# Optimization experiments

Hardware: AMD Instinct MI355X
Metric: run time of the kernel (lower is better)

## Reference

```python
import jax, jax.numpy as jnp
import numpy as np

SEQ_LEN = 720
PRED_LEN = 720
CHANNELS = 321
CUT_FREQ = 200
FREQ_OUT = 400  # int(cut_freq * (seq_len+pred_len)/seq_len)
LENGTH_RATIO = (SEQ_LEN + PRED_LEN) / SEQ_LEN  # 2.0
BATCH = 256


def setup_inputs() -> dict:
    key = jax.random.key(0)
    ks = jax.random.split(key, 8)
    scale = 1.0 / np.sqrt(CUT_FREQ)  # Linear-style init scale
    return {
        "x_enc": jax.random.normal(ks[0], (BATCH, SEQ_LEN, CHANNELS), dtype=jnp.float32),
        "x_mark_enc": jax.random.normal(ks[1], (BATCH, SEQ_LEN, 4), dtype=jnp.float32),
        "x_dec": jax.random.normal(ks[2], (BATCH, PRED_LEN, CHANNELS), dtype=jnp.float32),
        "x_mark_dec": jax.random.normal(ks[3], (BATCH, PRED_LEN, 4), dtype=jnp.float32),
        "Wr": jax.random.normal(ks[4], (CHANNELS, FREQ_OUT, CUT_FREQ), dtype=jnp.float32) * scale,
        "Wi": jax.random.normal(ks[5], (CHANNELS, FREQ_OUT, CUT_FREQ), dtype=jnp.float32) * scale,
        "br": jax.random.normal(ks[6], (CHANNELS, FREQ_OUT), dtype=jnp.float32) * scale,
        "bi": jax.random.normal(ks[7], (CHANNELS, FREQ_OUT), dtype=jnp.float32) * scale,
    }


def reference(x_enc, x_mark_enc, x_dec, x_mark_dec, Wr, Wi, br, bi):
    # RevIN-style normalization along time dim (unbiased variance, as torch.var)
    x_mean = jnp.mean(x_enc, axis=1, keepdims=True)                 # [B,1,C]
    x = x_enc - x_mean
    x_var = jnp.var(x, axis=1, keepdims=True, ddof=1)               # [B,1,C]
    x_stdev = jnp.sqrt(x_var + 1e-5)
    x = x / x_stdev

    # Low-pass in frequency domain
    x_freq = jnp.fft.rfft(x, axis=1)                                # [B, S//2+1, C] complex
    x_freq_low = x_freq[:, :CUT_FREQ, :]                            # [B, F_in, C]

    # Per-channel complex linear (the python loop over channels fused into one einsum)
    W = (Wr + 1j * Wi).astype(jnp.complex64)                        # [C, F_out, F_in]
    b = (br + 1j * bi).astype(jnp.complex64)                        # [C, F_out]
    out_freq = jnp.einsum('bfc,cof->boc', x_freq_low, W) + b.T[None]  # [B, F_out, C]

    # Back to time domain at the upsampled length
    total = SEQ_LEN + PRED_LEN
    out = jnp.fft.irfft(out_freq, n=total, axis=1) * LENGTH_RATIO   # [B, S+P, C]
    out = out[:, -PRED_LEN:, :]

    # De-normalize
    return out * x_stdev + x_mean
```

## Files before the change

kernel.cpp:

```cpp
#include <hip/hip_runtime.h>
#include <math.h>

#define SEQ    720
#define PRED   720
#define CH     321
#define FCUT   200
#define FOUT   400
#define NBATCH 256
#define NTOT   1440
#define KR     400
#define MC     800

typedef _Float16 f16;
typedef f16   f16x8 __attribute__((ext_vector_type(8)));
typedef float f32x4 __attribute__((ext_vector_type(4)));

static __device__ __forceinline__ f32x4 mfma16(f16x8 a, f16x8 b, f32x4 c) {
    return __builtin_amdgcn_mfma_f32_16x16x32_f16(a, b, c, 0, 0, 0);
}
static __device__ __forceinline__ f16 tof16(float v) { return (f16)v; }
static __device__ __forceinline__ ushort f16bits(f16 h) { return __builtin_bit_cast(unsigned short, h); }
static __device__ __forceinline__ f16 bits2f16(ushort u) { return __builtin_bit_cast(f16, u); }

__global__ void init_dmat(f16* __restrict__ Dh, f16* __restrict__ Dl) {
    int i = blockIdx.x * 256 + threadIdx.x;
    if (i >= KR * SEQ) return;
    int fp = i / SEQ, t = i % SEQ;
    int f = (fp < FCUT) ? fp : (fp - FCUT);
    int p = (f * t) % SEQ;
    float ang = (float)p * (6.28318530717958647692f / (float)SEQ);
    float v = (fp < FCUT) ? cosf(ang) : -sinf(ang);
    f16 h = tof16(v);
    Dh[i] = h;
    Dl[i] = tof16(v - (float)h);
}

__global__ void init_gmat(f16* __restrict__ Gh, f16* __restrict__ Gl) {
    int i = blockIdx.x * 256 + threadIdx.x;
    if (i >= SEQ * MC) return;
    int tp = i / MC, kp = i % MC;
    int t = tp + PRED;
    int k = (kp < FOUT) ? kp : (kp - FOUT);
    int p = (k * t) % NTOT;
    float ang = (float)p * (6.28318530717958647692f / (float)NTOT);
    const float s = 2.0f / (float)NTOT;
    float v;
    if (kp < FOUT) v = (k == 0) ? s : (2.0f * s * cosf(ang));
    else           v = (k == 0) ? 0.0f : (-2.0f * s * sinf(ang));
    f16 h = tof16(v);
    Gh[i] = h;
    Gl[i] = tof16(v - (float)h);
}

__global__ void stats_kernel(const float* __restrict__ x,
                             float* __restrict__ mean_bc,
                             float* __restrict__ rstd_bc,
                             float* __restrict__ stdev_bc) {
    int i = blockIdx.x * 256 + threadIdx.x;
    if (i >= NBATCH * CH) return;
    int b = i / CH, c = i % CH;
    const float* p = x + (size_t)b * SEQ * CH + c;
    float s = 0.f, ss = 0.f;
    for (int t = 0; t < SEQ; ++t) {
        float v = p[(size_t)t * CH];
        s += v; ss += v * v;
    }
    float mean = s / (float)SEQ;
    float var = fmaxf((ss - s * mean) / (float)(SEQ - 1), 0.f);
    float st = sqrtf(var + 1e-5f);
    mean_bc[i] = mean;
    stdev_bc[i] = st;
    rstd_bc[i] = 1.0f / st;
}

template<int MODE>
__global__ __launch_bounds__(256)
void gemm_mfma(const f16* __restrict__ Ahg,
               const f16* __restrict__ Alg,
               const void* __restrict__ Bg,
               void* __restrict__ Cg,
               const float* __restrict__ P0,
               const float* __restrict__ P1,
               const float* __restrict__ P2,
               const float* __restrict__ P3,
               int Bc, int b0, int gx, int gy)
{
    const int M   = (MODE == 0) ? KR : (MODE == 1) ? MC : SEQ;
    const int K   = (MODE == 0) ? SEQ : (MODE == 1) ? KR : MC;
    const int N   = (MODE == 0) ? CH : Bc;
    const int ldb = (MODE == 0) ? CH : Bc;
    const int ldc = (MODE == 0) ? CH : Bc;

    int orig = blockIdx.x;
    int q = (int)gridDim.x >> 3, r = (int)gridDim.x & 7, xcd = orig & 7;
    int id = (xcd < r ? xcd * (q + 1) : r * (q + 1) + (xcd - r) * q) + (orig >> 3);

    const int z   = id / (gx * gy);
    const int rem = id - z * (gx * gy);
    const int my  = rem / gx;
    const int mx  = rem - my * gx;
    const int m0  = mx * 128;
    const int n0  = my * 128;

    const void* Bp = nullptr; void* Cp = nullptr;
    const float* wrc = nullptr; const float* wic = nullptr;
    const float* mnp = nullptr; const float* rsp = nullptr;
    if (MODE == 0) {
        int b = b0 + z;
        Bp  = (const float*)Bg + (size_t)b * SEQ * CH;
        Cp  = (ushort*)Cg + (size_t)z * KR * CH;
        mnp = P0 + (size_t)b * CH;
        rsp = P1 + (size_t)b * CH;
    } else if (MODE == 1) {
        Bp  = (const ushort*)Bg + (size_t)z * KR * Bc;
        Cp  = (ushort*)Cg + (size_t)z * MC * Bc;
        wrc = P0 + (size_t)z * FOUT * FCUT;
        wic = P1 + (size_t)z * FOUT * FCUT;
    } else {
        Bp  = (const ushort*)Bg + (size_t)z * MC * Bc;
        Cp  = (float*)Cg + (size_t)z * SEQ * Bc;
    }

    __shared__ f16 Ah[4][128][8];
    __shared__ f16 Al[4][128][8];
    __shared__ f16 Bh[4][128][8];

    const int tid  = threadIdx.x;
    const int row  = tid & 127;
    const int half = tid >> 7;
    const int kloc = half * 16;

    const int lane = tid & 63;
    const int w    = tid >> 6;
    const int wm   = (w & 1) * 64;
    const int wn   = (w >> 1) * 64;
    const int fr   = lane & 15;
    const int kg   = lane >> 4;

    const int mg = m0 + row;
    const int ng = n0 + row;

    float mn = 0.f, rs = 0.f;
    if (MODE == 0 && ng < CH) { mn = mnp[ng]; rs = rsp[ng]; }

    f32x4 acc[4][4];
#pragma unroll
    for (int i = 0; i < 4; ++i)
#pragma unroll
        for (int j = 0; j < 4; ++j) acc[i][j] = (f32x4){0.f, 0.f, 0.f, 0.f};

    const int ksteps = (K + 31) / 32;
    for (int ks = 0; ks < ksteps; ++ks) {
        const int kb = ks * 32 + kloc;
        const bool kval = kb < K;

        if (MODE == 1) {
            float av[16];
            if (kval && mg < M) {
                const bool hi2 = mg >= FOUT;
                const int  o   = hi2 ? mg - FOUT : mg;
#pragma unroll
                for (int qd = 0; qd < 4; ++qd) {
                    int k = kb + qd * 4;
                    bool kb2 = k >= FCUT;
                    int  k2  = kb2 ? k - FCUT : k;
                    const float* basep = (hi2 != kb2) ? wic : wrc;
                    float4 v = *(const float4*)(basep + (size_t)o * FCUT + k2);
                    float sgn = (!hi2 && kb2) ? -1.f : 1.f;
                    av[qd * 4 + 0] = sgn * v.x; av[qd * 4 + 1] = sgn * v.y;
                    av[qd * 4 + 2] = sgn * v.z; av[qd * 4 + 3] = sgn * v.w;
                }
            } else {
#pragma unroll
                for (int u = 0; u < 16; ++u) av[u] = 0.f;
            }
#pragma unroll
            for (int ch = 0; ch < 2; ++ch) {
                f16x8 ah_, al_;
#pragma unroll
                for (int e = 0; e < 8; ++e) {
                    float va = av[ch * 8 + e];
                    f16 h = tof16(va);
                    ah_[e] = h;
                    al_[e] = tof16(va - (float)h);
                }
                *(f16x8*)&Ah[half * 2 + ch][row][0] = ah_;
                *(f16x8*)&Al[half * 2 + ch][row][0] = al_;
            }
        } else {
            f16x8 h0, h1, l0, l1;
            if (kval && mg < M) {
                const f16* ph = Ahg + (size_t)mg * K + kb;
                const f16* pl = Alg + (size_t)mg * K + kb;
                h0 = *(const f16x8*)(ph);
                h1 = *(const f16x8*)(ph + 8);
                l0 = *(const f16x8*)(pl);
                l1 = *(const f16x8*)(pl + 8);
            } else {
                h0 = (f16x8)(f16)0; h1 = (f16x8)(f16)0;
                l0 = (f16x8)(f16)0; l1 = (f16x8)(f16)0;
            }
            *(f16x8*)&Ah[half * 2 + 0][row][0] = h0;
            *(f16x8*)&Ah[half * 2 + 1][row][0] = h1;
            *(f16x8*)&Al[half * 2 + 0][row][0] = l0;
            *(f16x8*)&Al[half * 2 + 1][row][0] = l1;
        }

        {
            f16x8 b0, b1;
            if (kval && ng < N) {
                if (MODE == 0) {
                    const float* bp = (const float*)Bp + (size_t)kb * ldb + ng;
#pragma unroll
                    for (int u = 0; u < 8; ++u) b0[u] = tof16((bp[(size_t)u * ldb] - mn) * rs);
#pragma unroll
                    for (int u = 0; u < 8; ++u) b1[u] = tof16((bp[(size_t)(u + 8) * ldb] - mn) * rs);
                } else {
                    const ushort* bp = (const ushort*)Bp + (size_t)kb * ldb + ng;
#pragma unroll
                    for (int u = 0; u < 8; ++u) b0[u] = bits2f16(bp[(size_t)u * ldb]);
#pragma unroll
                    for (int u = 0; u < 8; ++u) b1[u] = bits2f16(bp[(size_t)(u + 8) * ldb]);
                }
            } else {
                b0 = (f16x8)(f16)0; b1 = (f16x8)(f16)0;
            }
            *(f16x8*)&Bh[half * 2 + 0][row][0] = b0;
            *(f16x8*)&Bh[half * 2 + 1][row][0] = b1;
        }
        __syncthreads();

        f16x8 a_h[4], a_l[4];
#pragma unroll
        for (int i = 0; i < 4; ++i) {
            a_h[i] = *(const f16x8*)&Ah[kg][wm + i * 16 + fr][0];
            a_l[i] = *(const f16x8*)&Al[kg][wm + i * 16 + fr][0];
        }
#pragma unroll
        for (int j = 0; j < 4; ++j) {
            f16x8 b_h = *(const f16x8*)&Bh[kg][wn + j * 16 + fr][0];
#pragma unroll
            for (int i = 0; i < 4; ++i) {
                acc[i][j] = mfma16(a_h[i], b_h, acc[i][j]);
                acc[i][j] = mfma16(a_l[i], b_h, acc[i][j]);
            }
        }
        __syncthreads();
    }

#pragma unroll
    for (int i = 0; i < 4; ++i) {
        const int mbase = m0 + wm + i * 16 + kg * 4;
#pragma unroll
        for (int r2 = 0; r2 < 4; ++r2) {
            const int mm = mbase + r2;
            if (mm >= M) continue;
            float bias = 0.f;
            if (MODE == 1)
                bias = (mm < FOUT) ? P2[(size_t)z * FOUT + mm]
                                   : P3[(size_t)z * FOUT + (mm - FOUT)];
#pragma unroll
            for (int j = 0; j < 4; ++j) {
                const int nn = n0 + wn + j * 16 + fr;
                if (nn < N) {
                    float v = acc[i][j][r2] + bias;
                    if (MODE == 2) ((float*)Cp)[(size_t)mm * ldc + nn] = v;
                    else           ((ushort*)Cp)[(size_t)mm * ldc + nn] = f16bits(tof16(v));
                }
            }
        }
    }
}

__global__ void transpose_bc(const ushort* __restrict__ in, ushort* __restrict__ out, int Bc) {
    __shared__ ushort tile[32][34];
    int f = blockIdx.x;
    int c0 = blockIdx.y * 32, b0 = blockIdx.z * 32;
    int tx = threadIdx.x, ty = threadIdx.y;
#pragma unroll
    for (int j = 0; j < 4; ++j) {
        int bb = b0 + ty + j * 8, cc = c0 + tx;
        if (bb < Bc && cc < CH)
            tile[ty + j * 8][tx] = in[(size_t)bb * KR * CH + (size_t)f * CH + cc];
    }
    __syncthreads();
#pragma unroll
    for (int j = 0; j < 4; ++j) {
        int cc = c0 + ty + j * 8, bb = b0 + tx;
        if (cc < CH && bb < Bc)
            out[(size_t)cc * KR * Bc + (size_t)f * Bc + bb] = tile[tx][ty + j * 8];
    }
}

__global__ void transpose_out(const float* __restrict__ outT,
                              const float* __restrict__ mean_bc,
                              const float* __restrict__ stdev_bc,
                              float* __restrict__ out, int b0, int Bc) {
    __shared__ float tile[32][33];
    int t = blockIdx.x;
    int c0 = blockIdx.y * 32, bb0 = blockIdx.z * 32;
    int tx = threadIdx.x, ty = threadIdx.y;
#pragma unroll
    for (int j = 0; j < 4; ++j) {
        int cc = c0 + ty + j * 8, bl = bb0 + tx;
        if (cc < CH && bl < Bc)
            tile[ty + j * 8][tx] = outT[(size_t)cc * SEQ * Bc + (size_t)t * Bc + bl];
    }
    __syncthreads();
#pragma unroll
    for (int j = 0; j < 4; ++j) {
        int cc = c0 + tx, bl = bb0 + ty + j * 8;
        if (cc < CH && bl < Bc) {
            int b = b0 + bl;
            size_t si = (size_t)b * CH + cc;
            out[(size_t)b * SEQ * CH + (size_t)t * CH + cc] =
                tile[tx][ty + j * 8] * stdev_bc[si] + mean_bc[si];
        }
    }
}

extern "C" void kernel_launch(void* const* d_in, const int* in_sizes, int n_in,
                              void* d_out, int out_size, void* d_ws, size_t ws_size,
                              hipStream_t stream) {
    const float* x_enc = (const float*)d_in[0];
    const float* Wr = (const float*)d_in[4];
    const float* Wi = (const float*)d_in[5];
    const float* br = (const float*)d_in[6];
    const float* bi = (const float*)d_in[7];
    float* out = (float*)d_out;

    auto alb = [](size_t x) { return (x + 255) & ~(size_t)255; };
    const size_t fixedB = 2 * alb((size_t)KR * SEQ * 2)
                        + 2 * alb((size_t)SEQ * MC * 2)
                        + 3 * alb((size_t)NBATCH * CH * 4);

    int Bc = NBATCH;
    while (Bc > 1) {
        size_t perB = 2 * alb((size_t)Bc * KR * CH * 2)
                    + alb((size_t)CH * MC * Bc * 2)
                    + alb((size_t)CH * SEQ * Bc * 4);
        if (fixedB + perB <= ws_size) break;
        Bc >>= 1;
    }

    char* wsb = (char*)d_ws;
    size_t off = 0;
    auto take = [&](size_t bytes) { size_t o = off; off += alb(bytes); return o; };
    f16*    Dh   = (f16*)(wsb + take((size_t)KR * SEQ * 2));
    f16*    Dl   = (f16*)(wsb + take((size_t)KR * SEQ * 2));
    f16*    Gh   = (f16*)(wsb + take((size_t)SEQ * MC * 2));
    f16*    Gl   = (f16*)(wsb + take((size_t)SEQ * MC * 2));
    float*  Mean = (float*)(wsb + take((size_t)NBATCH * CH * 4));
    float*  Rstd = (float*)(wsb + take((size_t)NBATCH * CH * 4));
    float*  Stdv = (float*)(wsb + take((size_t)NBATCH * CH * 4));
    ushort* Xb   = (ushort*)(wsb + take((size_t)Bc * KR * CH * 2));
    ushort* XT   = (ushort*)(wsb + take((size_t)Bc * KR * CH * 2));
    ushort* Fb   = (ushort*)(wsb + take((size_t)CH * MC * Bc * 2));
    float*  OT   = (float*)(wsb + take((size_t)CH * SEQ * Bc * 4));

    init_dmat<<<(KR * SEQ + 255) / 256, 256, 0, stream>>>(Dh, Dl);
    init_gmat<<<(SEQ * MC + 255) / 256, 256, 0, stream>>>(Gh, Gl);
    stats_kernel<<<(NBATCH * CH + 255) / 256, 256, 0, stream>>>(x_enc, Mean, Rstd, Stdv);

    const int nch = NBATCH / Bc;
    for (int ci = 0; ci < nch; ++ci) {
        int b0 = ci * Bc;

        {
            int gx = (KR + 127) / 128, gy = (CH + 127) / 128;
            int nb = gx * gy * Bc;
            gemm_mfma<0><<<nb, 256, 0, stream>>>(Dh, Dl, (const void*)x_enc, (void*)Xb,
                                                 Mean, Rstd, nullptr, nullptr,
                                                 Bc, b0, gx, gy);
        }

        dim3 gT1(KR, (CH + 31) / 32, (Bc + 31) / 32);
        transpose_bc<<<gT1, dim3(32, 8), 0, stream>>>(Xb, XT, Bc);

        {
            int gx = (MC + 127) / 128, gy = (Bc + 127) / 128;
            int nb = gx * gy * CH;
            gemm_mfma<1><<<nb, 256, 0, stream>>>(nullptr, nullptr, (const void*)XT, (void*)Fb,
                                                 Wr, Wi, br, bi,
                                                 Bc, 0, gx, gy);
        }

        {
            int gx = (SEQ + 127) / 128, gy = (Bc + 127) / 128;
            int nb = gx * gy * CH;
            gemm_mfma<2><<<nb, 256, 0, stream>>>(Gh, Gl, (const void*)Fb, (void*)OT,
                                                 nullptr, nullptr, nullptr, nullptr,
                                                 Bc, 0, gx, gy);
        }

        dim3 gT3(SEQ, (CH + 31) / 32, (Bc + 31) / 32);
        transpose_out<<<gT3, dim3(32, 8), 0, stream>>>(OT, Mean, Stdv, out, b0, Bc);
    }
}
```

Before: 1.707 ms.

## Double-buffer LDS tiles and prefetch next K-step into registers

After: 1.697 ms. No clear change (-0.6%).

```diff
diff --git a/kernel.cpp b/kernel.cpp
--- a/kernel.cpp
+++ b/kernel.cpp
@@ -121,14 +121,13 @@
         Cp  = (float*)Cg + (size_t)z * SEQ * Bc;
     }
 
-    __shared__ f16 Ah[4][128][8];
-    __shared__ f16 Al[4][128][8];
-    __shared__ f16 Bh[4][128][8];
+    __shared__ f16 AhS[2][4][128][8];
+    __shared__ f16 AlS[2][4][128][8];
+    __shared__ f16 BhS[2][4][128][8];
 
     const int tid  = threadIdx.x;
     const int row  = tid & 127;
     const int half = tid >> 7;
-    const int kloc = half * 16;
 
     const int lane = tid & 63;
     const int w    = tid >> 6;
@@ -149,13 +148,17 @@
 #pragma unroll
         for (int j = 0; j < 4; ++j) acc[i][j] = (f32x4){0.f, 0.f, 0.f, 0.f};
 
+    f16x8 rah0, rah1, ral0, ral1;
+    float  rav[16];
+    float  rbf[16];
+    ushort rbu[16];
+
     const int ksteps = (K + 31) / 32;
-    for (int ks = 0; ks < ksteps; ++ks) {
-        const int kb = ks * 32 + kloc;
+
+    auto LOAD = [&](int ks) {
+        const int kb = ks * 32 + half * 16;
         const bool kval = kb < K;
-
         if (MODE == 1) {
-            float av[16];
             if (kval && mg < M) {
                 const bool hi2 = mg >= FOUT;
                 const int  o   = hi2 ? mg - FOUT : mg;
@@ -167,85 +170,117 @@
                     const float* basep = (hi2 != kb2) ? wic : wrc;
                     float4 v = *(const float4*)(basep + (size_t)o * FCUT + k2);
                     float sgn = (!hi2 && kb2) ? -1.f : 1.f;
-                    av[qd * 4 + 0] = sgn * v.x; av[qd * 4 + 1] = sgn * v.y;
-                    av[qd * 4 + 2] = sgn * v.z; av[qd * 4 + 3] = sgn * v.w;
+                    rav[qd * 4 + 0] = sgn * v.x; rav[qd * 4 + 1] = sgn * v.y;
+                    rav[qd * 4 + 2] = sgn * v.z; rav[qd * 4 + 3] = sgn * v.w;
                 }
             } else {
 #pragma unroll
-                for (int u = 0; u < 16; ++u) av[u] = 0.f;
-            }
+                for (int u = 0; u < 16; ++u) rav[u] = 0.f;
+            }
+        } else {
+            if (kval && mg < M) {
+                const f16* ph = Ahg + (size_t)mg * K + kb;
+                const f16* pl = Alg + (size_t)mg * K + kb;
+                rah0 = *(const f16x8*)(ph);
+                rah1 = *(const f16x8*)(ph + 8);
+                ral0 = *(const f16x8*)(pl);
+                ral1 = *(const f16x8*)(pl + 8);
+            } else {
+                rah0 = (f16x8)(f16)0; rah1 = (f16x8)(f16)0;
+                ral0 = (f16x8)(f16)0; ral1 = (f16x8)(f16)0;
+            }
+        }
+        if (kval && ng < N) {
+            if (MODE == 0) {
+                const float* bp = (const float*)Bp + (size_t)kb * ldb + ng;
+#pragma unroll
+                for (int u = 0; u < 16; ++u) rbf[u] = bp[(size_t)u * ldb];
+            } else {
+                const ushort* bp = (const ushort*)Bp + (size_t)kb * ldb + ng;
+#pragma unroll
+                for (int u = 0; u < 16; ++u) rbu[u] = bp[(size_t)u * ldb];
+            }
+        } else {
+            if (MODE == 0) {
+#pragma unroll
+                for (int u = 0; u < 16; ++u) rbf[u] = 0.f;
+            } else {
+#pragma unroll
+                for (int u = 0; u < 16; ++u) rbu[u] = 0;
+            }
+        }
+    };
+
+    auto STORE = [&](int pb) {
+        if (MODE == 1) {
 #pragma unroll
             for (int ch = 0; ch < 2; ++ch) {
                 f16x8 ah_, al_;
 #pragma unroll
                 for (int e = 0; e < 8; ++e) {
-                    float va = av[ch * 8 + e];
+                    float va = rav[ch * 8 + e];
                     f16 h = tof16(va);
                     ah_[e] = h;
                     al_[e] = tof16(va - (float)h);
                 }
-                *(f16x8*)&Ah[half * 2 + ch][row][0] = ah_;
-                *(f16x8*)&Al[half * 2 + ch][row][0] = al_;
+                *(f16x8*)&AhS[pb][half * 2 + ch][row][0] = ah_;
+                *(f16x8*)&AlS[pb][half * 2 + ch][row][0] = al_;
             }
         } else {
-            f16x8 h0, h1, l0, l1;
-            if (kval && mg < M) {
-                const f16* ph = Ahg + (size_t)mg * K + kb;
-                const f16* pl = Alg + (size_t)mg * K + kb;
-                h0 = *(const f16x8*)(ph);
-                h1 = *(const f16x8*)(ph + 8);
-                l0 = *(const f16x8*)(pl);
-                l1 = *(const f16x8*)(pl + 8);
+            *(f16x8*)&AhS[pb][half * 2 + 0][row][0] = rah0;
+            *(f16x8*)&AhS[pb][half * 2 + 1][row][0] = rah1;
+            *(f16x8*)&AlS[pb][half * 2 + 0][row][0] = ral0;
+            *(f16x8*)&AlS[pb][half * 2 + 1][row][0] = ral1;
+        }
+        {
+            f16x8 b0_, b1_;
+            if (MODE == 0) {
+#pragma unroll
+                for (int u = 0; u < 8; ++u) b0_[u] = tof16((rbf[u] - mn) * rs);
+#pragma unroll
+                for (int u = 0; u < 8; ++u) b1_[u] = tof16((rbf[u + 8] - mn) * rs);
             } else {
-                h0 = (f16x8)(f16)0; h1 = (f16x8)(f16)0;
-                l0 = (f16x8)(f16)0; l1 = (f16x8)(f16)0;
-            }
-            *(f16x8*)&Ah[half * 2 + 0][row][0] = h0;
-            *(f16x8*)&Ah[half * 2 + 1][row][0] = h1;
-            *(f16x8*)&Al[half * 2 + 0][row][0] = l0;
-            *(f16x8*)&Al[half * 2 + 1][row][0] = l1;
-        }
-
-        {
-            f16x8 b0, b1;
-            if (kval && ng < N) {
-                if (MODE == 0) {
-                    const float* bp = (const float*)Bp + (size_t)kb * ldb + ng;
-#pragma unroll
-                    for (int u = 0; u < 8; ++u) b0[u] = tof16((bp[(size_t)u * ldb] - mn) * rs);
-#pragma unroll
-                    for (int u = 0; u < 8; ++u) b1[u] = tof16((bp[(size_t)(u + 8) * ldb] - mn) * rs);
-                } else {
-                    const ushort* bp = (const ushort*)Bp + (size_t)kb * ldb + ng;
-#pragma unroll
-                    for (int u = 0; u < 8; ++u) b0[u] = bits2f16(bp[(size_t)u * ldb]);
-#pragma unroll
-                    for (int u = 0; u < 8; ++u) b1[u] = bits2f16(bp[(size_t)(u + 8) * ldb]);
-                }
-            } else {
-                b0 = (f16x8)(f16)0; b1 = (f16x8)(f16)0;
-            }
-            *(f16x8*)&Bh[half * 2 + 0][row][0] = b0;
-            *(f16x8*)&Bh[half * 2 + 1][row][0] = b1;
-        }
-        __syncthreads();
-
+#pragma unroll
+                for (int u = 0; u < 8; ++u) b0_[u] = bits2f16(rbu[u]);
+#pragma unroll
+                for (int u = 0; u < 8; ++u) b1_[u] = bits2f16(rbu[u + 8]);
+            }
+            *(f16x8*)&BhS[pb][half * 2 + 0][row][0] = b0_;
+            *(f16x8*)&BhS[pb][half * 2 + 1][row][0] = b1_;
+        }
+    };
+
+    auto COMPUTE = [&](int pb) {
         f16x8 a_h[4], a_l[4];
 #pragma unroll
         for (int i = 0; i < 4; ++i) {
-            a_h[i] = *(const f16x8*)&Ah[kg][wm + i * 16 + fr][0];
-            a_l[i] = *(const f16x8*)&Al[kg][wm + i * 16 + fr][0];
-        }
+            a_h[i] = *(const f16x8*)&AhS[pb][kg][wm + i * 16 + fr][0];
+            a_l[i] = *(const f16x8*)&AlS[pb][kg][wm + i * 16 + fr][0];
+        }
+        __builtin_amdgcn_s_setprio(1);
 #pragma unroll
         for (int j = 0; j < 4; ++j) {
-            f16x8 b_h = *(const f16x8*)&Bh[kg][wn + j * 16 + fr][0];
+            f16x8 b_h = *(const f16x8*)&BhS[pb][kg][wn + j * 16 + fr][0];
 #pragma unroll
             for (int i = 0; i < 4; ++i) {
                 acc[i][j] = mfma16(a_h[i], b_h, acc[i][j]);
                 acc[i][j] = mfma16(a_l[i], b_h, acc[i][j]);
             }
         }
+        __builtin_amdgcn_s_setprio(0);
+    };
+
+    LOAD(0);
+    STORE(0);
+    __syncthreads();
+
+    int cur = 0;
+    for (int ks = 0; ks < ksteps; ++ks) {
+        LOAD(ks + 1);
+        COMPUTE(cur);
+        STORE(cur ^ 1);
         __syncthreads();
+        cur ^= 1;
     }
 
 #pragma unroll
```
